# Performance work log

Measured on AMD Instinct MI355X. Metric: run time of the kernel, lower is better.

## Reference

```python
import jax, jax.numpy as jnp
import numpy as np

D_MODEL = 2048
NUM_HEADS = 16
HEAD_DIM = D_MODEL // NUM_HEADS


def _rotary(x, head_dim):
    # x: (..., T, head_dim). Matches torch module: half-split rotation.
    T = x.shape[-2]
    pos = jnp.arange(T, dtype=jnp.float32)[:, None]              # (T,1)
    dim = jnp.arange(head_dim // 2, dtype=jnp.float32)[None, :]  # (1,hd/2)
    angle = pos * (1.0 / jnp.power(10000.0, 2.0 * dim / head_dim))
    cos = jnp.cos(angle)  # (T, hd/2), broadcasts over leading dims
    sin = jnp.sin(angle)
    x1 = x[..., : head_dim // 2]
    x2 = x[..., head_dim // 2:]
    return jnp.concatenate([x1 * cos - x2 * sin, x2 * cos + x1 * sin], axis=-1)


def setup_inputs() -> dict:
    key = jax.random.key(0)
    ks = jax.random.split(key, 9)
    B, T, D, H, HD = 2, 2048, D_MODEL, NUM_HEADS, HEAD_DIM
    s = 1.0 / np.sqrt(D)
    return {
        "x": jax.random.normal(ks[0], (B, T, D), jnp.float32),
        "Wq": jax.random.normal(ks[1], (D, D), jnp.float32) * s,
        "bq": jnp.zeros((D,), jnp.float32),
        "Wk": jax.random.normal(ks[2], (D, HD), jnp.float32) * s,
        "bk": jnp.zeros((HD,), jnp.float32),
        "Wv": jax.random.normal(ks[3], (D, HD), jnp.float32) * s,
        "bv": jnp.zeros((HD,), jnp.float32),
        "Wo": jax.random.normal(ks[4], (D, D), jnp.float32) * s,
        "bo": jnp.zeros((D,), jnp.float32),
    }


def reference(x, Wq, bq, Wk, bk, Wv, bv, Wo, bo):
    B, T, D = x.shape
    H, HD = NUM_HEADS, HEAD_DIM
    q = (x @ Wq + bq).reshape(B, T, H, HD).transpose(0, 2, 1, 3)  # (B,H,T,hd)
    k = (x @ Wk + bk)[:, None]                                    # (B,1,T,hd)
    v = (x @ Wv + bv)[:, None]                                    # (B,1,T,hd)
    q = _rotary(q, HD)
    k = _rotary(k, HD)
    scores = jnp.einsum("bhqd,bhkd->bhqk", q, jnp.broadcast_to(k, (B, 1, T, HD))) / jnp.sqrt(jnp.float32(HD))
    attn = jax.nn.softmax(scores, axis=-1)                        # (B,H,T,T)
    ctx = jnp.einsum("bhqk,bhkd->bhqd", attn, jnp.broadcast_to(v, (B, 1, T, HD)))
    ctx = ctx.transpose(0, 2, 1, 3).reshape(B, T, D)
    return ctx @ Wo + bo
```

## Files before the change

### kernel.cpp

```cpp
#include <hip/hip_runtime.h>
#include <math.h>

#define T_SEQ  2048
#define DMODEL 2048
#define NHEADS 16
#define HDIM   128
#define MROWS  4096

typedef __attribute__((ext_vector_type(8)))  __bf16 bf16x8;
typedef __attribute__((ext_vector_type(4)))  __bf16 bf16x4;
typedef __attribute__((ext_vector_type(4)))  float  f32x4;
typedef __attribute__((ext_vector_type(16))) float  f32x16;
typedef __attribute__((ext_vector_type(4)))  unsigned int uint32x4;

#define GLOBAL_AS __attribute__((address_space(1)))
#define LDS_AS    __attribute__((address_space(3)))
__device__ __forceinline__ void async_copy16(const __bf16* g, __bf16* l) {
  __builtin_amdgcn_global_load_lds((const GLOBAL_AS void*)g, (LDS_AS void*)l, 16, 0, 0);
}

__device__ __forceinline__ unsigned int pack_bf16_2(float a, float b) {
  __bf16 x = (__bf16)a, y = (__bf16)b;
  unsigned short ux = __builtin_bit_cast(unsigned short, x);
  unsigned short uy = __builtin_bit_cast(unsigned short, y);
  return (unsigned int)ux | ((unsigned int)uy << 16);
}

__global__ __launch_bounds__(256) void prep_kernel(
    const float* __restrict__ x,
    const float* __restrict__ Wq, const float* __restrict__ Wk,
    const float* __restrict__ Wv, const float* __restrict__ Wo,
    float2* __restrict__ rope, __bf16* __restrict__ xb,
    __bf16* __restrict__ wqkvt, __bf16* __restrict__ wot)
{
  __shared__ float t[32][33];
  const int bid = blockIdx.x;
  const int tid = threadIdx.x;

  if (bid < 512) {
    int idx = bid*256 + tid;
    int d = idx & 63, pos = idx >> 6;
    double freq = pow(10000.0, -(double)d / 64.0);
    double ang = (double)pos * freq;
    rope[idx] = make_float2((float)cos(ang), (float)sin(ang));
    return;
  }
  if (bid < 512 + 8192) {
    int i = (bid - 512)*256 + tid;
    float4 v = ((const float4*)x)[i];
    bf16x4 o = { (__bf16)v.x, (__bf16)v.y, (__bf16)v.z, (__bf16)v.w };
    *(bf16x4*)(xb + (size_t)i*4) = o;
    return;
  }
  const int lb = bid - (512 + 8192);
  const int by = lb / 136;
  const int bx = lb - by*136;
  const float* src; __bf16* dst; int istride, c0, orow;
  if (bx < 64)       { src = Wq; istride = 2048; c0 = bx*32;      orow = c0;        dst = wqkvt; }
  else if (bx < 68)  { src = Wk; istride = 128;  c0 = (bx-64)*32; orow = 2048 + c0; dst = wqkvt; }
  else if (bx < 72)  { src = Wv; istride = 128;  c0 = (bx-68)*32; orow = 2176 + c0; dst = wqkvt; }
  else               { src = Wo; istride = 2048; c0 = (bx-72)*32; orow = c0;        dst = wot; }
  const int tx = tid & 31, ty = tid >> 5;
  const int r0 = by*32;
#pragma unroll
  for (int i = 0; i < 4; ++i)
    t[ty + i*8][tx] = src[(size_t)(r0 + ty + i*8)*istride + c0 + tx];
  __syncthreads();
#pragma unroll
  for (int i = 0; i < 4; ++i)
    dst[(size_t)(orow + ty + i*8)*2048 + r0 + tx] = (__bf16)t[tx][ty + i*8];
}

__global__ __launch_bounds__(256) void gemm_qkv_fused(
    const __bf16* __restrict__ A,
    const __bf16* __restrict__ Bt,
    const float* __restrict__ bq, const float* __restrict__ bk,
    const float* __restrict__ bv,
    const float2* __restrict__ rope,
    __bf16* __restrict__ qrb,
    __bf16* __restrict__ kbb,
    __bf16* __restrict__ vtb,
    float qscale)
{
  __shared__ __bf16 As[128*32];
  __shared__ __bf16 Bs[128*32];
  const int orig = blockIdx.x;
  const int wgid = (orig & 7)*72 + (orig >> 3);
  const int by = wgid & 31, bx = wgid >> 5;
  const int tid = threadIdx.x;
  const int lane = tid & 63, wave = tid >> 6;
  const int quad = lane >> 4, l16 = lane & 15;
  const int m0 = (wave >> 1)*64, n0 = (wave & 1)*32;
  const int row0 = by*128, col0 = bx*128;
  const int srow = lane >> 2, scol = (lane & 3)*8;

  f32x4 acc[4][4];
#pragma unroll
  for (int i = 0; i < 4; ++i)
#pragma unroll
    for (int j = 0; j < 4; ++j) acc[i][j] = (f32x4){0.f,0.f,0.f,0.f};

  const __bf16* Ag = A  + (size_t)(row0 + wave*32 + srow)*DMODEL + scol;
  const __bf16* Bg = Bt + (size_t)(col0 + wave*32 + srow)*DMODEL + scol;
  __bf16* AsW = &As[wave*1024];
  __bf16* BsW = &Bs[wave*1024];

  for (int kk = 0; kk < DMODEL; kk += 32) {
    __syncthreads();
    async_copy16(Ag + kk,                     AsW);
    async_copy16(Ag + kk + (size_t)16*DMODEL, AsW + 512);
    async_copy16(Bg + kk,                     BsW);
    async_copy16(Bg + kk + (size_t)16*DMODEL, BsW + 512);
    __syncthreads();
    bf16x8 af[4], bfr[4];
#pragma unroll
    for (int i = 0; i < 4; ++i)
      af[i] = *(const bf16x8*)&As[(m0 + i*16 + l16)*32 + quad*8];
#pragma unroll
    for (int j = 0; j < 4; ++j) {
      const int cb = n0 + (j & 1)*16 + (j >> 1)*64;
      bfr[j] = *(const bf16x8*)&Bs[(cb + l16)*32 + quad*8];
    }
#pragma unroll
    for (int i = 0; i < 4; ++i)
#pragma unroll
      for (int j = 0; j < 4; ++j)
        acc[i][j] = __builtin_amdgcn_mfma_f32_16x16x32_bf16(af[i], bfr[j], acc[i][j], 0,0,0);
  }

  if (bx == 17) {
#pragma unroll
    for (int j = 0; j < 2; ++j) {
      const int d = n0 + j*16 + l16;
      const float b1 = bv[d], b2 = bv[d + 64];
#pragma unroll
      for (int i = 0; i < 4; ++i) {
        const int rg = row0 + m0 + i*16 + quad*4;
        const int bb = rg >> 11, t0 = rg & (T_SEQ-1);
        bf16x4 p1, p2;
#pragma unroll
        for (int r = 0; r < 4; ++r) {
          p1[r] = (__bf16)(acc[i][j][r]   + b1);
          p2[r] = (__bf16)(acc[i][j+2][r] + b2);
        }
        *(bf16x4*)&vtb[((size_t)bb*128 + d)*T_SEQ + t0]      = p1;
        *(bf16x4*)&vtb[((size_t)bb*128 + d + 64)*T_SEQ + t0] = p2;
      }
    }
    return;
  }

  const float* bias_p; float scale; __bf16* obase; int ostride;
  if (bx < 16)      { bias_p = bq + bx*128; scale = qscale;
                      obase = qrb + bx*128; ostride = 2048; }
  else              { bias_p = bk; scale = 1.f;
                      obase = kbb; ostride = 128; }

#pragma unroll
  for (int j = 0; j < 2; ++j) {
    const int d = n0 + j*16 + l16;
    const float b1 = bias_p[d], b2 = bias_p[d + 64];
#pragma unroll
    for (int i = 0; i < 4; ++i) {
      const int rl = m0 + i*16 + quad*4;
#pragma unroll
      for (int r = 0; r < 4; ++r) {
        const int rg = row0 + rl + r;
        const float x1 = acc[i][j][r]   + b1;
        const float x2 = acc[i][j+2][r] + b2;
        float2 cs = rope[(size_t)(rg & (T_SEQ-1))*64 + d];
        obase[(size_t)rg*ostride + d]      = (__bf16)((x1*cs.x - x2*cs.y)*scale);
        obase[(size_t)rg*ostride + d + 64] = (__bf16)((x2*cs.x + x1*cs.y)*scale);
      }
    }
  }
}

__global__ __launch_bounds__(256) void gemm_bf16_t128(
    const __bf16* __restrict__ A, const __bf16* __restrict__ Bt,
    const float* __restrict__ bias, float* __restrict__ C,
    int M, int N, int K)
{
  __shared__ __bf16 As[128*32];
  __shared__ __bf16 Bs[128*32];
  const int nwg = gridDim.x;
  const int rowTiles = M >> 7;
  const int q = nwg >> 3;
  const int orig = blockIdx.x;
  const int wgid = (orig & 7)*q + (orig >> 3);
  const int by = wgid % rowTiles, bx = wgid / rowTiles;
  const int tid = threadIdx.x;
  const int lane = tid & 63, wave = tid >> 6;
  const int quad = lane >> 4, l16 = lane & 15;
  const int m0 = (wave & 1)*64, n0 = (wave >> 1)*64;
  const int row0 = by*128, col0 = bx*128;
  const int srow = lane >> 2, scol = (lane & 3)*8;

  f32x4 acc[4][4];
#pragma unroll
  for (int i = 0; i < 4; ++i)
#pragma unroll
    for (int j = 0; j < 4; ++j) acc[i][j] = (f32x4){0.f,0.f,0.f,0.f};

  const __bf16* Ag = A  + (size_t)(row0 + wave*32 + srow)*K + scol;
  const __bf16* Bg = Bt + (size_t)(col0 + wave*32 + srow)*K + scol;
  __bf16* AsW = &As[wave*1024];
  __bf16* BsW = &Bs[wave*1024];

  for (int kk = 0; kk < K; kk += 32) {
    __syncthreads();
    async_copy16(Ag + kk,              AsW);
    async_copy16(Ag + kk + (size_t)16*K, AsW + 512);
    async_copy16(Bg + kk,              BsW);
    async_copy16(Bg + kk + (size_t)16*K, BsW + 512);
    __syncthreads();
    bf16x8 af[4], bfr[4];
#pragma unroll
    for (int i = 0; i < 4; ++i)
      af[i] = *(const bf16x8*)&As[(m0 + i*16 + l16)*32 + quad*8];
#pragma unroll
    for (int j = 0; j < 4; ++j)
      bfr[j] = *(const bf16x8*)&Bs[(n0 + j*16 + l16)*32 + quad*8];
#pragma unroll
    for (int i = 0; i < 4; ++i)
#pragma unroll
      for (int j = 0; j < 4; ++j)
        acc[i][j] = __builtin_amdgcn_mfma_f32_16x16x32_bf16(af[i], bfr[j], acc[i][j], 0,0,0);
  }
#pragma unroll
  for (int j = 0; j < 4; ++j) {
    const int ccol = col0 + n0 + j*16 + l16;
    const float bvv = bias[ccol];
#pragma unroll
    for (int i = 0; i < 4; ++i) {
      const int crow = row0 + m0 + i*16 + quad*4;
#pragma unroll
      for (int r = 0; r < 4; ++r)
        C[(size_t)(crow + r)*N + ccol] = acc[i][j][r] + bvv;
    }
  }
}

#define KSTR 136
#define VSTR 72
__global__ __launch_bounds__(256) void mqa_attn_mfma(
    const __bf16* __restrict__ qb,
    const __bf16* __restrict__ kb,
    const __bf16* __restrict__ vt,
    __bf16* __restrict__ ctx)
{
  __shared__ __bf16 Ks[64*KSTR];
  __shared__ __bf16 Vs[128*VSTR];
  __shared__ float  Linv[128];
  const int tid = threadIdx.x, lane = tid & 63, wave = tid >> 6;
  const int h5 = lane >> 5, l32 = lane & 31;
  const int h = blockIdx.y, b = blockIdx.z;
  const int qbase = blockIdx.x*128 + wave*32;

  bf16x8 qf[8];
  const __bf16* qp = qb + ((size_t)b*T_SEQ + qbase + l32)*DMODEL + h*HDIM;
#pragma unroll
  for (int ds = 0; ds < 8; ++ds) qf[ds] = *(const bf16x8*)(qp + ds*16 + h5*8);

  f32x16 oacc[4];
#pragma unroll
  for (int g = 0; g < 4; ++g)
#pragma unroll
    for (int r = 0; r < 16; ++r) oacc[g][r] = 0.f;
  float lsum = 0.f;

  const __bf16* kbase = kb + (size_t)b*T_SEQ*HDIM;
  const __bf16* vbase = vt + (size_t)b*HDIM*T_SEQ;

  for (int kt = 0; kt < T_SEQ/64; ++kt) {
    __syncthreads();
#pragma unroll
    for (int i = 0; i < 4; ++i) {
      int idx = i*256 + tid;
      int key = idx >> 4, c = idx & 15;
      *(bf16x8*)&Ks[key*KSTR + c*8] =
          *(const bf16x8*)(kbase + (size_t)(kt*64 + key)*HDIM + c*8);
    }
#pragma unroll
    for (int i = 0; i < 4; ++i) {
      int idx = i*256 + tid;
      int d = idx >> 3, c = idx & 7;
      *(bf16x8*)&Vs[d*VSTR + c*8] =
          *(const bf16x8*)(vbase + (size_t)d*T_SEQ + kt*64 + c*8);
    }
    __syncthreads();

    f32x16 sacc[2];
#pragma unroll
    for (int kg = 0; kg < 2; ++kg) {
#pragma unroll
      for (int r = 0; r < 16; ++r) sacc[kg][r] = 0.f;
      __builtin_amdgcn_s_setprio(1);
#pragma unroll
      for (int ds = 0; ds < 8; ++ds) {
        bf16x8 kf = *(const bf16x8*)&Ks[(kg*32 + l32)*KSTR + ds*16 + h5*8];
        sacc[kg] = __builtin_amdgcn_mfma_f32_32x32x16_bf16(kf, qf[ds], sacc[kg], 0,0,0);
      }
      __builtin_amdgcn_s_setprio(0);
    }

    bf16x8 pf[4];
#pragma unroll
    for (int kg = 0; kg < 2; ++kg) {
      unsigned int w[8];
#pragma unroll
      for (int m = 0; m < 8; ++m) {
        float p0 = __builtin_amdgcn_exp2f(sacc[kg][2*m]);
        float p1 = __builtin_amdgcn_exp2f(sacc[kg][2*m+1]);
        lsum += p0; lsum += p1;
        w[m] = pack_bf16_2(p0, p1);
      }
#pragma unroll
      for (int kss = 0; kss < 2; ++kss) {
        auto s1 = __builtin_amdgcn_permlane32_swap(w[4*kss+0], w[4*kss+2], false, false);
        auto s2 = __builtin_amdgcn_permlane32_swap(w[4*kss+1], w[4*kss+3], false, false);
        uint32x4 u = (uint32x4){ s1[0], s2[0], s1[1], s2[1] };
        pf[kg*2 + kss] = __builtin_bit_cast(bf16x8, u);
      }
    }

    __builtin_amdgcn_s_setprio(1);
#pragma unroll
    for (int ks = 0; ks < 4; ++ks) {
#pragma unroll
      for (int g = 0; g < 4; ++g) {
        bf16x8 vf = *(const bf16x8*)&Vs[(g*32 + l32)*VSTR + ks*16 + h5*8];
        oacc[g] = __builtin_amdgcn_mfma_f32_32x32x16_bf16(pf[ks], vf, oacc[g], 0,0,0);
      }
    }
    __builtin_amdgcn_s_setprio(0);
  }

  lsum += __shfl_xor(lsum, 32);
  if (h5 == 0) Linv[wave*32 + l32] = 1.f / lsum;
  __asm__ volatile("s_waitcnt lgkmcnt(0)" ::: "memory");

  __bf16* op = ctx + ((size_t)b*T_SEQ + qbase)*DMODEL + h*HDIM + l32;
#pragma unroll
  for (int r1 = 0; r1 < 4; ++r1) {
    float4 iv = *(const float4*)&Linv[wave*32 + r1*8 + h5*4];
#pragma unroll
    for (int r0 = 0; r0 < 4; ++r0) {
      int qrow = r1*8 + h5*4 + r0;
#pragma unroll
      for (int g = 0; g < 4; ++g)
        op[(size_t)qrow*DMODEL + g*32] = (__bf16)(oacc[g][r1*4 + r0] * (&iv.x)[r0]);
    }
  }
}

extern "C" void kernel_launch(void* const* d_in, const int* in_sizes, int n_in,
                              void* d_out, int out_size, void* d_ws, size_t ws_size,
                              hipStream_t stream) {
  const float* x  = (const float*)d_in[0];
  const float* Wq = (const float*)d_in[1];
  const float* bq = (const float*)d_in[2];
  const float* Wk = (const float*)d_in[3];
  const float* bk = (const float*)d_in[4];
  const float* Wv = (const float*)d_in[5];
  const float* bv = (const float*)d_in[6];
  const float* Wo = (const float*)d_in[7];
  const float* bo = (const float*)d_in[8];
  float* out = (float*)d_out;

  uint8_t* ws = (uint8_t*)d_ws;
  __bf16* qrb  = (__bf16*)(ws);
  __bf16* xb   = (__bf16*)(ws + 16777216);
  __bf16* wqkvt= (__bf16*)(ws + 33554432);
  __bf16* wot  = (__bf16*)(ws + 42991616);
  __bf16* kbb  = (__bf16*)(ws + 51380224);
  __bf16* vtb  = (__bf16*)(ws + 53477376);
  float2* rope = (float2*)(ws + 54525952);

  const float qscale = 1.4426950408889634f * 0.08838834764831845f;

  prep_kernel<<<dim3(17408), 256, 0, stream>>>(x, Wq, Wk, Wv, Wo, rope, xb, wqkvt, wot);

  gemm_qkv_fused<<<dim3(576), 256, 0, stream>>>(
      xb, wqkvt, bq, bk, bv, rope, qrb, kbb, vtb, qscale);

  mqa_attn_mfma<<<dim3(16,16,2), 256, 0, stream>>>(qrb, kbb, vtb, xb);

  gemm_bf16_t128<<<dim3(512), 256, 0, stream>>>(xb, wot, bo, out, MROWS, DMODEL, DMODEL);
}
```

Baseline: 335.7 us.

## Double-buffer LDS tiles in QKV and output GEMMs, drop XCD block remap

Both GEMM kernels now use two LDS buffers per operand. The next K-slice is prefetched asynchronously while MFMAs run on the current one, which cuts the per-iteration barriers from two to one so load latency can overlap compute. The XCD-aware workgroup index remapping is also removed in favour of a plain 2D grid, which may reduce L2 locality across chiplets. LDS use per block doubles, which could limit occupancy.

```diff
diff --git a/kernel.cpp b/kernel.cpp
--- a/kernel.cpp
+++ b/kernel.cpp
@@ -82,11 +82,9 @@
     __bf16* __restrict__ vtb,
     float qscale)
 {
-  __shared__ __bf16 As[128*32];
-  __shared__ __bf16 Bs[128*32];
-  const int orig = blockIdx.x;
-  const int wgid = (orig & 7)*72 + (orig >> 3);
-  const int by = wgid & 31, bx = wgid >> 5;
+  __shared__ __bf16 As[2][128*32];
+  __shared__ __bf16 Bs[2][128*32];
+  const int bx = blockIdx.x, by = blockIdx.y;
   const int tid = threadIdx.x;
   const int lane = tid & 63, wave = tid >> 6;
   const int quad = lane >> 4, l16 = lane & 15;
@@ -102,30 +100,39 @@
 
   const __bf16* Ag = A  + (size_t)(row0 + wave*32 + srow)*DMODEL + scol;
   const __bf16* Bg = Bt + (size_t)(col0 + wave*32 + srow)*DMODEL + scol;
-  __bf16* AsW = &As[wave*1024];
-  __bf16* BsW = &Bs[wave*1024];
-
+  const int woff = wave*1024;
+
+  async_copy16(Ag,                     &As[0][woff]);
+  async_copy16(Ag + (size_t)16*DMODEL, &As[0][woff + 512]);
+  async_copy16(Bg,                     &Bs[0][woff]);
+  async_copy16(Bg + (size_t)16*DMODEL, &Bs[0][woff + 512]);
+  __syncthreads();
+
+  int cur = 0;
   for (int kk = 0; kk < DMODEL; kk += 32) {
-    __syncthreads();
-    async_copy16(Ag + kk,                     AsW);
-    async_copy16(Ag + kk + (size_t)16*DMODEL, AsW + 512);
-    async_copy16(Bg + kk,                     BsW);
-    async_copy16(Bg + kk + (size_t)16*DMODEL, BsW + 512);
-    __syncthreads();
+    if (kk + 32 < DMODEL) {
+      const int nb = cur ^ 1;
+      async_copy16(Ag + kk + 32,                     &As[nb][woff]);
+      async_copy16(Ag + kk + 32 + (size_t)16*DMODEL, &As[nb][woff + 512]);
+      async_copy16(Bg + kk + 32,                     &Bs[nb][woff]);
+      async_copy16(Bg + kk + 32 + (size_t)16*DMODEL, &Bs[nb][woff + 512]);
+    }
     bf16x8 af[4], bfr[4];
 #pragma unroll
     for (int i = 0; i < 4; ++i)
-      af[i] = *(const bf16x8*)&As[(m0 + i*16 + l16)*32 + quad*8];
+      af[i] = *(const bf16x8*)&As[cur][(m0 + i*16 + l16)*32 + quad*8];
 #pragma unroll
     for (int j = 0; j < 4; ++j) {
       const int cb = n0 + (j & 1)*16 + (j >> 1)*64;
-      bfr[j] = *(const bf16x8*)&Bs[(cb + l16)*32 + quad*8];
+      bfr[j] = *(const bf16x8*)&Bs[cur][(cb + l16)*32 + quad*8];
     }
 #pragma unroll
     for (int i = 0; i < 4; ++i)
 #pragma unroll
       for (int j = 0; j < 4; ++j)
         acc[i][j] = __builtin_amdgcn_mfma_f32_16x16x32_bf16(af[i], bfr[j], acc[i][j], 0,0,0);
+    __syncthreads();
+    cur ^= 1;
   }
 
   if (bx == 17) {
@@ -181,19 +188,13 @@
     const float* __restrict__ bias, float* __restrict__ C,
     int M, int N, int K)
 {
-  __shared__ __bf16 As[128*32];
-  __shared__ __bf16 Bs[128*32];
-  const int nwg = gridDim.x;
-  const int rowTiles = M >> 7;
-  const int q = nwg >> 3;
-  const int orig = blockIdx.x;
-  const int wgid = (orig & 7)*q + (orig >> 3);
-  const int by = wgid % rowTiles, bx = wgid / rowTiles;
+  __shared__ __bf16 As[2][128*32];
+  __shared__ __bf16 Bs[2][128*32];
   const int tid = threadIdx.x;
   const int lane = tid & 63, wave = tid >> 6;
   const int quad = lane >> 4, l16 = lane & 15;
   const int m0 = (wave & 1)*64, n0 = (wave >> 1)*64;
-  const int row0 = by*128, col0 = bx*128;
+  const int row0 = blockIdx.y*128, col0 = blockIdx.x*128;
   const int srow = lane >> 2, scol = (lane & 3)*8;
 
   f32x4 acc[4][4];
@@ -204,28 +205,37 @@
 
   const __bf16* Ag = A  + (size_t)(row0 + wave*32 + srow)*K + scol;
   const __bf16* Bg = Bt + (size_t)(col0 + wave*32 + srow)*K + scol;
-  __bf16* AsW = &As[wave*1024];
-  __bf16* BsW = &Bs[wave*1024];
-
+  const int woff = wave*1024;
+
+  async_copy16(Ag,                &As[0][woff]);
+  async_copy16(Ag + (size_t)16*K, &As[0][woff + 512]);
+  async_copy16(Bg,                &Bs[0][woff]);
+  async_copy16(Bg + (size_t)16*K, &Bs[0][woff + 512]);
+  __syncthreads();
+
+  int cur = 0;
   for (int kk = 0; kk < K; kk += 32) {
-    __syncthreads();
-    async_copy16(Ag + kk,              AsW);
-    async_copy16(Ag + kk + (size_t)16*K, AsW + 512);
-    async_copy16(Bg + kk,              BsW);
-    async_copy16(Bg + kk + (size_t)16*K, BsW + 512);
-    __syncthreads();
+    if (kk + 32 < K) {
+      const int nb = cur ^ 1;
+      async_copy16(Ag + kk + 32,                &As[nb][woff]);
+      async_copy16(Ag + kk + 32 + (size_t)16*K, &As[nb][woff + 512]);
+      async_copy16(Bg + kk + 32,                &Bs[nb][woff]);
+      async_copy16(Bg + kk + 32 + (size_t)16*K, &Bs[nb][woff + 512]);
+    }
     bf16x8 af[4], bfr[4];
 #pragma unroll
     for (int i = 0; i < 4; ++i)
-      af[i] = *(const bf16x8*)&As[(m0 + i*16 + l16)*32 + quad*8];
+      af[i] = *(const bf16x8*)&As[cur][(m0 + i*16 + l16)*32 + quad*8];
 #pragma unroll
     for (int j = 0; j < 4; ++j)
-      bfr[j] = *(const bf16x8*)&Bs[(n0 + j*16 + l16)*32 + quad*8];
+      bfr[j] = *(const bf16x8*)&Bs[cur][(n0 + j*16 + l16)*32 + quad*8];
 #pragma unroll
     for (int i = 0; i < 4; ++i)
 #pragma unroll
       for (int j = 0; j < 4; ++j)
         acc[i][j] = __builtin_amdgcn_mfma_f32_16x16x32_bf16(af[i], bfr[j], acc[i][j], 0,0,0);
+    __syncthreads();
+    cur ^= 1;
   }
 #pragma unroll
   for (int j = 0; j < 4; ++j) {
@@ -381,10 +391,10 @@
 
   prep_kernel<<<dim3(17408), 256, 0, stream>>>(x, Wq, Wk, Wv, Wo, rope, xb, wqkvt, wot);
 
-  gemm_qkv_fused<<<dim3(576), 256, 0, stream>>>(
+  gemm_qkv_fused<<<dim3(18,32), 256, 0, stream>>>(
       xb, wqkvt, bq, bk, bv, rope, qrb, kbb, vtb, qscale);
 
   mqa_attn_mfma<<<dim3(16,16,2), 256, 0, stream>>>(qrb, kbb, vtb, xb);
 
-  gemm_bf16_t128<<<dim3(512), 256, 0, stream>>>(xb, wot, bo, out, MROWS, DMODEL, DMODEL);
-}
+  gemm_bf16_t128<<<dim3(16,32), 256, 0, stream>>>(xb, wot, bo, out, MROWS, DMODEL, DMODEL);
+}
```

Result: no change. 334.3 us (-0.4%).
